# Optimization experiments

Measured on AMD Instinct MI355X. Metric: run time of the kernel, lower is better.

## Reference

```python
import jax, jax.numpy as jnp
import numpy as np

EPS = 0.001  # additive floor applied after relu, as in the torch code


def setup_inputs() -> dict:
    key = jax.random.key(0)
    kA, kB, kW = jax.random.split(key, 3)
    M, N, C, H, W = 512, 64, 128, 8, 8
    A = jax.random.normal(kA, (M, C, H, W), dtype=jnp.float32)
    B = jax.random.normal(kB, (N, C, H, W), dtype=jnp.float32)
    Wg = jax.random.normal(kW, (C, C), dtype=jnp.float32) * 0.01  # Wg.data.normal_(0.0, 0.01)
    return {"A": A, "B": B, "Wg": Wg}


def reference(A, B, Wg):
    # Faithful vectorization of MIMOcom.get_source_dst_max(A, B, dir=True).
    # Torch loops i,j over HxW: B0 = B[:, i, j, :]; G = B0 @ Wg;
    # combination[m, n, p] = sum_c A[m, p, c] * G[n, c]; running max over (i, j).
    M, C, H, W = A.shape
    N = B.shape[0]
    P = H * W
    Af = jnp.transpose(A, (0, 2, 3, 1)).reshape(M, P, C)  # [M, P, C]
    Bf = jnp.transpose(B, (0, 2, 3, 1)).reshape(N, P, C)  # [N, Q, C]
    G = Bf @ Wg                                           # [N, Q, D]
    scores = jnp.einsum('mpd,nqd->mnpq', Af, G)           # [M, N, P, Q]
    comb_max = scores.max(axis=-1)                        # max over B positions q
    return jax.nn.relu(comb_max) + EPS                    # [M, N, P]
```

## Files before the change

### kernel.cpp

```cpp
#include <hip/hip_runtime.h>
#include <hip/hip_bf16.h>
#include <stdint.h>

typedef __attribute__((ext_vector_type(8))) short bf16x8;
typedef __attribute__((ext_vector_type(16))) float f32x16;
using bf16 = __hip_bfloat16;

static constexpr int Mdim = 512;
static constexpr int Ndim = 64;
static constexpr int Cdim = 128;
static constexpr int Pdim = 64;
static constexpr float EPS_ADD = 0.001f;

#define SB0 __builtin_amdgcn_sched_barrier(0)

__device__ __forceinline__ void gll16(const void* gsrc, void* ldst) {
    const __attribute__((address_space(1))) unsigned int* g =
        (const __attribute__((address_space(1))) unsigned int*)gsrc;
    __attribute__((address_space(3))) unsigned int* l =
        (__attribute__((address_space(3))) unsigned int*)(uintptr_t)ldst;
    __builtin_amdgcn_global_load_lds(g, l, 16, 0, 0);
}

__global__ void prep_kernel(const float* __restrict__ A, const float* __restrict__ B,
                            const float* __restrict__ Wg,
                            bf16* __restrict__ Afrag, bf16* __restrict__ Gfrag) {
    __shared__ float lds[128 * 65];
    const int t = threadIdx.x;

    if (blockIdx.x < 512) {
        const int m = blockIdx.x;
        const float* __restrict__ Am = A + (size_t)m * (Cdim * Pdim);
#pragma unroll
        for (int i = 0; i < 8; ++i) {
            int v = t + i * 256;
            int gidx = v * 4;
            int c = gidx >> 6, p = gidx & 63;
            float4 val = *reinterpret_cast<const float4*>(Am + gidx);
            float* dst = &lds[c * 65 + p];
            dst[0] = val.x; dst[1] = val.y; dst[2] = val.z; dst[3] = val.w;
        }
        __syncthreads();

        unsigned* __restrict__ dst32 = (unsigned*)(Afrag + (size_t)m * 8192);
#pragma unroll
        for (int i = 0; i < 16; ++i) {
            int pr = t + i * 256;
            int p = pr >> 6;
            int c = (pr & 63) << 1;
            float f0 = lds[c * 65 + p];
            float f1 = lds[(c + 1) * 65 + p];
            union { bf16 hh[2]; unsigned u; } pk;
            pk.hh[0] = __float2bfloat16(f0);
            pk.hh[1] = __float2bfloat16(f1);
            int h = p >> 5, l31 = p & 31;
            int ks = c >> 4, hi = (c >> 3) & 1, e = c & 7;
            dst32[h * 2048 + ks * 256 + hi * 128 + l31 * 4 + (e >> 1)] = pk.u;
        }
    } else {
        const int nb = blockIdx.x - 512;
        const int n  = nb >> 2;
        const int q0 = (nb & 3) * 16;
        const float* __restrict__ Bn = B + (size_t)n * (Cdim * Pdim);
#pragma unroll
        for (int i = 0; i < 8; ++i) {
            int v = t + i * 256;
            int gidx = v * 4;
            int c = gidx >> 6, q = gidx & 63;
            float4 val = *reinterpret_cast<const float4*>(Bn + gidx);
            float* dst = &lds[c * 65 + q];
            dst[0] = val.x; dst[1] = val.y; dst[2] = val.z; dst[3] = val.w;
        }
        __syncthreads();

        const int d  = t & 127;
        const int qb = q0 + (t >> 7) * 8;
        float acc[8] = {0.f, 0.f, 0.f, 0.f, 0.f, 0.f, 0.f, 0.f};
        for (int c = 0; c < 128; ++c) {
            float w = Wg[c * 128 + d];
#pragma unroll
            for (int qi = 0; qi < 8; ++qi)
                acc[qi] = fmaf(lds[c * 65 + qb + qi], w, acc[qi]);
        }
        bf16* __restrict__ gdst = Gfrag + (size_t)n * 8192;
        const int ks = d >> 4, hi = (d >> 3) & 1, e = d & 7;
#pragma unroll
        for (int qi = 0; qi < 8; ++qi) {
            int q = qb + qi;
            int qt = q >> 5, l31 = q & 31;
            gdst[qt * 4096 + ks * 512 + hi * 256 + l31 * 8 + e] = __float2bfloat16(acc[qi]);
        }
    }
}

__global__ __launch_bounds__(256, 3)
void gemm_max_kernel(const bf16* __restrict__ Afrag, const bf16* __restrict__ Gfrag,
                     float* __restrict__ out) {
    __shared__ bf16 sG[2][8192];
    const int tid  = threadIdx.x;
    const int lane = tid & 63;
    const int wv   = tid >> 6;
    const int mi = wv >> 1, h = wv & 1;
    const int l31 = lane & 31, hi = lane >> 5;
    const int mg = blockIdx.x & 127;
    const int bn = blockIdx.x >> 7;
    const int m0 = mg * 4 + mi * 2;

    bf16x8 a[2][8];
#pragma unroll
    for (int u = 0; u < 2; ++u) {
        const bf16* Ap = Afrag + (size_t)(m0 + u) * 8192 + h * 4096 + lane * 8;
#pragma unroll
        for (int ks = 0; ks < 8; ++ks)
            a[u][ks] = *reinterpret_cast<const bf16x8*>(Ap + ks * 512);
    }
    asm volatile("" ::: "memory");

    const char* Gsrc = (const char*)(Gfrag + (size_t)(bn * 8) * 8192);
    auto stageG = [&](int s) {
        char* dst = (char*)&sG[s & 1][0];
        const char* src = Gsrc + (size_t)s * 16384;
#pragma unroll
        for (int i = 0; i < 4; ++i) {
            int f = (i * 256 + tid) * 16;
            gll16(src + f, dst + f);
        }
    };

    const f32x16 z16 = {0.f,0.f,0.f,0.f,0.f,0.f,0.f,0.f,0.f,0.f,0.f,0.f,0.f,0.f,0.f,0.f};
    f32x16 acc0, acc1;
    bf16x8 gf0[8], gf1[8];

    auto ldgf = [&](bf16x8 (&g)[8], const char* base) {
#pragma unroll
        for (int ks = 0; ks < 8; ++ks)
            g[ks] = *reinterpret_cast<const bf16x8*>(base + ks * 1024);
    };
    auto mmcl = [&](const bf16x8 (&gf)[8]) {
        __builtin_amdgcn_s_setprio(1);
        acc0 = __builtin_amdgcn_mfma_f32_32x32x16_bf16(gf[0], a[0][0], z16, 0, 0, 0);
        acc1 = __builtin_amdgcn_mfma_f32_32x32x16_bf16(gf[0], a[1][0], z16, 0, 0, 0);
#pragma unroll
        for (int ks = 1; ks < 8; ++ks) {
            acc0 = __builtin_amdgcn_mfma_f32_32x32x16_bf16(gf[ks], a[0][ks], acc0, 0, 0, 0);
            acc1 = __builtin_amdgcn_mfma_f32_32x32x16_bf16(gf[ks], a[1][ks], acc1, 0, 0, 0);
        }
        __builtin_amdgcn_s_setprio(0);
    };
    auto red16 = [&](const f32x16& v) -> float {
        float x0 = fmaxf(v[0], v[1]),  x1 = fmaxf(v[2], v[3]);
        float x2 = fmaxf(v[4], v[5]),  x3 = fmaxf(v[6], v[7]);
        float x4 = fmaxf(v[8], v[9]),  x5 = fmaxf(v[10], v[11]);
        float x6 = fmaxf(v[12], v[13]), x7 = fmaxf(v[14], v[15]);
        x0 = fmaxf(x0, x1); x2 = fmaxf(x2, x3);
        x4 = fmaxf(x4, x5); x6 = fmaxf(x6, x7);
        return fmaxf(fmaxf(x0, x2), fmaxf(x4, x6));
    };

#define BODY(S, WV, DOSTAGE)                                                  \
    if (DOSTAGE) stageG((S) + 1);                                             \
    asm volatile("s_waitcnt vmcnt(" #WV ")" ::: "memory");                    \
    __builtin_amdgcn_s_barrier(); SB0;                                        \
    ldgf(gf0, (const char*)&sG[(S) & 1][0] + lane * 16);                      \
    ldgf(gf1, (const char*)&sG[(S) & 1][0] + 8192 + lane * 16);               \
    mmcl(gf0);                                                                \
    {                                                                         \
        float t0 = red16(acc0), t1 = red16(acc1);                             \
        mmcl(gf1);                                                            \
        t0 = fmaxf(t0, red16(acc0)); t1 = fmaxf(t1, red16(acc1));             \
        t0 = fmaxf(t0, __shfl_xor(t0, 32));                                   \
        t1 = fmaxf(t1, __shfl_xor(t1, 32));                                   \
        const int n = bn * 8 + (S);                                           \
        const float sv = hi ? t1 : t0;                                        \
        out[(size_t)(m0 + hi) * 4096 + n * 64 + h * 32 + l31] =               \
            fmaxf(sv, 0.f) + EPS_ADD;                                         \
    }

    stageG(0);
    asm volatile("s_waitcnt vmcnt(0)" ::: "memory");
    __builtin_amdgcn_s_barrier(); SB0;

    BODY(0, 4, 1)
    BODY(1, 5, 1)
    BODY(2, 5, 1)
    BODY(3, 5, 1)
    BODY(4, 5, 1)
    BODY(5, 5, 1)
    BODY(6, 5, 1)
    BODY(7, 1, 0)
#undef BODY
}

extern "C" void kernel_launch(void* const* d_in, const int* in_sizes, int n_in,
                              void* d_out, int out_size, void* d_ws, size_t ws_size,
                              hipStream_t stream) {
    const float* A  = (const float*)d_in[0];
    const float* B  = (const float*)d_in[1];
    const float* Wg = (const float*)d_in[2];
    float* out = (float*)d_out;

    bf16* Afrag = (bf16*)d_ws;
    bf16* Gfrag = (bf16*)((char*)d_ws + (size_t)Mdim * Pdim * Cdim * sizeof(bf16));

    prep_kernel<<<768, 256, 0, stream>>>(A, B, Wg, Afrag, Gfrag);
    gemm_max_kernel<<<1024, 256, 0, stream>>>(Afrag, Gfrag, out);
}
```

Baseline: 51.61 us.

## Load all four G tiles up front, halve per-block N and double grid

```diff
diff --git a/kernel.cpp b/kernel.cpp
--- a/kernel.cpp
+++ b/kernel.cpp
@@ -11,8 +11,6 @@
 static constexpr int Cdim = 128;
 static constexpr int Pdim = 64;
 static constexpr float EPS_ADD = 0.001f;
-
-#define SB0 __builtin_amdgcn_sched_barrier(0)
 
 __device__ __forceinline__ void gll16(const void* gsrc, void* ldst) {
     const __attribute__((address_space(1))) unsigned int* g =
@@ -93,10 +91,10 @@
     }
 }
 
-__global__ __launch_bounds__(256, 3)
+__global__ __launch_bounds__(256, 2)
 void gemm_max_kernel(const bf16* __restrict__ Afrag, const bf16* __restrict__ Gfrag,
                      float* __restrict__ out) {
-    __shared__ bf16 sG[2][8192];
+    __shared__ bf16 sG[4][8192];
     const int tid  = threadIdx.x;
     const int lane = tid & 63;
     const int wv   = tid >> 6;
@@ -114,18 +112,17 @@
         for (int ks = 0; ks < 8; ++ks)
             a[u][ks] = *reinterpret_cast<const bf16x8*>(Ap + ks * 512);
     }
-    asm volatile("" ::: "memory");
-
-    const char* Gsrc = (const char*)(Gfrag + (size_t)(bn * 8) * 8192);
-    auto stageG = [&](int s) {
-        char* dst = (char*)&sG[s & 1][0];
-        const char* src = Gsrc + (size_t)s * 16384;
+    {
+        const char* Gsrc = (const char*)(Gfrag + (size_t)(bn * 4) * 8192);
 #pragma unroll
-        for (int i = 0; i < 4; ++i) {
+        for (int i = 0; i < 16; ++i) {
             int f = (i * 256 + tid) * 16;
-            gll16(src + f, dst + f);
+            gll16(Gsrc + f, (char*)sG + f);
         }
-    };
+    }
+    asm volatile("s_waitcnt vmcnt(0)" ::: "memory");
+    __builtin_amdgcn_s_barrier();
+    __builtin_amdgcn_sched_barrier(0);
 
     const f32x16 z16 = {0.f,0.f,0.f,0.f,0.f,0.f,0.f,0.f,0.f,0.f,0.f,0.f,0.f,0.f,0.f,0.f};
     f32x16 acc0, acc1;
@@ -137,7 +134,6 @@
             g[ks] = *reinterpret_cast<const bf16x8*>(base + ks * 1024);
     };
     auto mmcl = [&](const bf16x8 (&gf)[8]) {
-        __builtin_amdgcn_s_setprio(1);
         acc0 = __builtin_amdgcn_mfma_f32_32x32x16_bf16(gf[0], a[0][0], z16, 0, 0, 0);
         acc1 = __builtin_amdgcn_mfma_f32_32x32x16_bf16(gf[0], a[1][0], z16, 0, 0, 0);
 #pragma unroll
@@ -145,7 +141,6 @@
             acc0 = __builtin_amdgcn_mfma_f32_32x32x16_bf16(gf[ks], a[0][ks], acc0, 0, 0, 0);
             acc1 = __builtin_amdgcn_mfma_f32_32x32x16_bf16(gf[ks], a[1][ks], acc1, 0, 0, 0);
         }
-        __builtin_amdgcn_s_setprio(0);
     };
     auto red16 = [&](const f32x16& v) -> float {
         float x0 = fmaxf(v[0], v[1]),  x1 = fmaxf(v[2], v[3]);
@@ -157,38 +152,23 @@
         return fmaxf(fmaxf(x0, x2), fmaxf(x4, x6));
     };
 
-#define BODY(S, WV, DOSTAGE)                                                  \
-    if (DOSTAGE) stageG((S) + 1);                                             \
-    asm volatile("s_waitcnt vmcnt(" #WV ")" ::: "memory");                    \
-    __builtin_amdgcn_s_barrier(); SB0;                                        \
-    ldgf(gf0, (const char*)&sG[(S) & 1][0] + lane * 16);                      \
-    ldgf(gf1, (const char*)&sG[(S) & 1][0] + 8192 + lane * 16);               \
-    mmcl(gf0);                                                                \
-    {                                                                         \
-        float t0 = red16(acc0), t1 = red16(acc1);                             \
-        mmcl(gf1);                                                            \
-        t0 = fmaxf(t0, red16(acc0)); t1 = fmaxf(t1, red16(acc1));             \
-        t0 = fmaxf(t0, __shfl_xor(t0, 32));                                   \
-        t1 = fmaxf(t1, __shfl_xor(t1, 32));                                   \
-        const int n = bn * 8 + (S);                                           \
-        const float sv = hi ? t1 : t0;                                        \
-        out[(size_t)(m0 + hi) * 4096 + n * 64 + h * 32 + l31] =               \
-            fmaxf(sv, 0.f) + EPS_ADD;                                         \
+#pragma unroll
+    for (int s = 0; s < 4; ++s) {
+        const char* gb = (const char*)sG + s * 16384 + lane * 16;
+        ldgf(gf0, gb);
+        ldgf(gf1, gb + 8192);
+        mmcl(gf0);
+        float t0 = red16(acc0), t1 = red16(acc1);
+        mmcl(gf1);
+        t0 = fmaxf(t0, red16(acc0));
+        t1 = fmaxf(t1, red16(acc1));
+        t0 = fmaxf(t0, __shfl_xor(t0, 32));
+        t1 = fmaxf(t1, __shfl_xor(t1, 32));
+        const int n = bn * 4 + s;
+        const float sv = hi ? t1 : t0;
+        out[(size_t)(m0 + hi) * 4096 + n * 64 + h * 32 + l31] =
+            fmaxf(sv, 0.f) + EPS_ADD;
     }
-
-    stageG(0);
-    asm volatile("s_waitcnt vmcnt(0)" ::: "memory");
-    __builtin_amdgcn_s_barrier(); SB0;
-
-    BODY(0, 4, 1)
-    BODY(1, 5, 1)
-    BODY(2, 5, 1)
-    BODY(3, 5, 1)
-    BODY(4, 5, 1)
-    BODY(5, 5, 1)
-    BODY(6, 5, 1)
-    BODY(7, 1, 0)
-#undef BODY
 }
 
 extern "C" void kernel_launch(void* const* d_in, const int* in_sizes, int n_in,
@@ -203,5 +183,5 @@
     bf16* Gfrag = (bf16*)((char*)d_ws + (size_t)Mdim * Pdim * Cdim * sizeof(bf16));
 
     prep_kernel<<<768, 256, 0, stream>>>(A, B, Wg, Afrag, Gfrag);
-    gemm_max_kernel<<<1024, 256, 0, stream>>>(Afrag, Gfrag, out);
+    gemm_max_kernel<<<2048, 256, 0, stream>>>(Afrag, Gfrag, out);
 }
```

After: 45.40 us. 1.14x faster.
